# Kernel tuning notes

Measured on AMD Instinct MI355X. Metric: run time of the kernel, lower is better.

The kernel has to match this reference:

```python
import jax, jax.numpy as jnp
import numpy as np

B, D, O, K = 8192, 256, 256, 16


def setup_inputs() -> dict:
    key = jax.random.key(0)
    k1, k2, k3, k4 = jax.random.split(key, 4)
    x = jax.random.normal(k1, (B, D), dtype=jnp.float32)
    # learned params
    values = jax.random.uniform(k2, (O, D, K), dtype=jnp.float32, minval=-0.05, maxval=0.05)
    skip_w = jax.random.normal(k3, (O, D), dtype=jnp.float32) * (1.0 / np.sqrt(D))
    skip_b = jax.random.uniform(k4, (O,), dtype=jnp.float32, minval=-1.0, maxval=1.0) / np.sqrt(D)
    # fixed buffer (non-trainable)
    grid = jnp.linspace(-1.0, 1.0, K).astype(jnp.float32)
    return {"x": x, "values": values, "skip_w": skip_w, "skip_b": skip_b, "grid": grid}


def reference(x, values, skip_w, skip_b, grid):
    # x: [B, D]; values: [O, D, K]; grid: [K]
    num_knots = grid.shape[0]
    xc = jnp.clip(x, -1.0, 1.0)
    # torch.bucketize(x, grid) (right=False) == searchsorted side='left'
    right = jnp.searchsorted(grid, xc, side="left")            # [B, D]
    left = jnp.clip(right - 1, 0, num_knots - 2)               # [B, D]
    right = left + 1
    g0 = grid[left]
    g1 = grid[right]
    w = (xc - g0) / (g1 - g0 + 1e-12)                          # [B, D]
    # sparse linear-interp coefficients over knots: 2 nonzeros per (b, d)
    coeff = (1.0 - w)[..., None] * jax.nn.one_hot(left, num_knots, dtype=xc.dtype) \
          + w[..., None] * jax.nn.one_hot(right, num_knots, dtype=xc.dtype)  # [B, D, K]
    # y[b,o] = sum_d sum_k coeff[b,d,k] * values[o,d,k]  (== per-dim gather+interp+accumulate)
    y = jnp.einsum("bdk,odk->bo", coeff, values)
    y = y + xc @ skip_w.T + skip_b
    return y
```

## Files before the change

### kernel.cpp

```cpp
#include <hip/hip_runtime.h>
#include <hip/hip_bf16.h>
#include <stdint.h>


#define D_DIM  256
#define O_DIM  256
#define BM     128
#define BK     64
#define KS     4
#define ITERS  16
#define NTHR   512

typedef __attribute__((ext_vector_type(8))) short bf16x8;
typedef __attribute__((ext_vector_type(4))) float f32x4;

__global__ __launch_bounds__(256) void kan_prep(
    const float* __restrict__ values,
    const float* __restrict__ skip_w,
    const float* __restrict__ gknots,
    unsigned short* __restrict__ Vp)
{
    int tid = blockIdx.x * blockDim.x + threadIdx.x;
    int e = tid * 8;
    int o = e >> 12;
    int kflat = e & 4095;
    float sw = skip_w[(o << 8) | (kflat >> 4)];
    int kmod = kflat & 15;

    const float4* vp4 = reinterpret_cast<const float4*>(values + e);
    float4 v0 = vp4[0], v1 = vp4[1];
    float f[8] = {v0.x, v0.y, v0.z, v0.w, v1.x, v1.y, v1.z, v1.w};
    unsigned int w[4];
#pragma unroll
    for (int j = 0; j < 4; ++j) {
        float2 ab;
        ab.x = f[2*j]     + gknots[kmod + 2*j]     * sw;
        ab.y = f[2*j + 1] + gknots[kmod + 2*j + 1] * sw;
        __hip_bfloat162 p2 = __float22bfloat162_rn(ab);
        __builtin_memcpy(&w[j], &p2, 4);
    }
    size_t c = (size_t)(kflat >> 3) * 256 + (size_t)o;
    *reinterpret_cast<uint4*>(Vp + c * 8) = make_uint4(w[0], w[1], w[2], w[3]);
}

__global__ __launch_bounds__(NTHR, 2) void kan_gemm(
    const float* __restrict__ x,
    const unsigned short* __restrict__ Vp,
    float* __restrict__ part,
    float* __restrict__ out)
{
    __shared__ unsigned short As[2][BM * BK];

    const int t    = threadIdx.x;
    const int lane = t & 63;
    const int wid  = t >> 6;
    const int wm   = wid >> 2;
    const int wn   = wid & 3;
    const int l15  = lane & 15;
    const int lhi  = lane >> 4;

    const int bid = (int)blockIdx.x;
    const int m8  = bid & 7;
    const int ks  = (bid >> 3) & 3;
    const int mhi = bid >> 5;
    const int mt  = m8 + 8 * mhi;
    const int bm0 = mt * BM;
    const size_t kc0 = (size_t)ks * 128;

    const int ar = t >> 2;
    const int ad = t & 3;
    const float* xp = x + (size_t)(bm0 + ar) * D_DIM + ks * 64 + ad;

    char* arow[2] = { (char*)&As[0][0] + ar * 128, (char*)&As[1][0] + ar * 128 };
    const int ca = ((2 * ad)     ^ (ar & 7)) * 16;
    const int cb = ((2 * ad + 1) ^ (ar & 7)) * 16;

    auto stageA = [&](int buf, float xv) {
        float xc = fminf(1.f, fmaxf(-1.f, xv));
        float tt = (xc + 1.f) * 7.5f;
        int li = (int)tt;
        li = li > 14 ? 14 : li;
        float w1 = tt - (float)li;
        float2 cw; cw.x = 1.f - w1; cw.y = w1;
        __hip_bfloat162 p2 = __float22bfloat162_rn(cw);
        unsigned int pk;
        __builtin_memcpy(&pk, &p2, 4);
        unsigned long long w64 = (unsigned long long)pk << ((li & 1) * 16);
        unsigned int lo = (unsigned int)w64;
        unsigned int hi = (unsigned int)(w64 >> 32);
        int jl = li >> 1;
        unsigned int wd[8];
#pragma unroll
        for (int j = 0; j < 8; ++j)
            wd[j] = (j == jl) ? lo : ((j == jl + 1) ? hi : 0u);
        char* a = arow[buf];
        *reinterpret_cast<uint4*>(a + ca) = make_uint4(wd[0], wd[1], wd[2], wd[3]);
        *reinterpret_cast<uint4*>(a + cb) = make_uint4(wd[4], wd[5], wd[6], wd[7]);
    };

    #define LOADB(BG, KT)                                                      \
        {                                                                      \
            const unsigned short* _b =                                         \
                Vp + (kc0 + (size_t)(KT) * 8) * 2048;                          \
            _Pragma("unroll")                                                  \
            for (int kh = 0; kh < 2; ++kh)                                     \
                _Pragma("unroll")                                              \
                for (int ni = 0; ni < 4; ++ni) {                               \
                    int n = wn * 64 + ni * 16 + l15;                           \
                    BG[kh * 4 + ni] = *reinterpret_cast<const bf16x8*>(        \
                        _b + ((size_t)((kh * 4 + lhi) * 256 + n)) * 8);        \
                }                                                              \
        }

    f32x4 acc[4][4] = {};
    bf16x8 bgA[8], bgB[8];

    int abyte[4], a7[4];
#pragma unroll
    for (int mi = 0; mi < 4; ++mi) {
        int m = wm * 64 + mi * 16 + l15;
        abyte[mi] = m * 128;
        a7[mi] = m & 7;
    }

    float xnxt = xp[0];
    LOADB(bgA, 0);
    stageA(0, xnxt);
    xnxt = xp[4];
    asm volatile("s_waitcnt lgkmcnt(0)" ::: "memory");
    __builtin_amdgcn_s_barrier();
    __builtin_amdgcn_sched_barrier(0);

    #define ITERBODY(KT, CUR, BGC, BGN)                                        \
        {                                                                      \
            const bool last = (KT) == ITERS - 1;                               \
            if (!last) LOADB(BGN, (KT) + 1);                                   \
            const char* Ab = (const char*)&As[CUR][0];                         \
            bf16x8 af[4];                                                      \
                                                                   \
            _Pragma("unroll")                                                  \
            for (int mi = 0; mi < 4; ++mi)                                     \
                af[mi] = *reinterpret_cast<const bf16x8*>(                     \
                    Ab + abyte[mi] + ((lhi ^ a7[mi]) << 4));                   \
            __builtin_amdgcn_s_setprio(1);                                     \
            _Pragma("unroll")                                                  \
            for (int mi = 0; mi < 4; ++mi)                                     \
                _Pragma("unroll")                                              \
                for (int ni = 0; ni < 4; ++ni)                                 \
                    acc[mi][ni] = __builtin_amdgcn_mfma_f32_16x16x32_bf16(     \
                        af[mi], BGC[ni], acc[mi][ni], 0, 0, 0);                \
            __builtin_amdgcn_s_setprio(0);                                     \
                                      \
            if (!last) {                                                       \
                stageA((CUR) ^ 1, xnxt);                                       \
                if ((KT) + 2 < ITERS) xnxt = xp[((KT) + 2) * 4];               \
            }                                                                  \
                                                                   \
            _Pragma("unroll")                                                  \
            for (int mi = 0; mi < 4; ++mi)                                     \
                af[mi] = *reinterpret_cast<const bf16x8*>(                     \
                    Ab + abyte[mi] + (((4 + lhi) ^ a7[mi]) << 4));             \
            __builtin_amdgcn_s_setprio(1);                                     \
            _Pragma("unroll")                                                  \
            for (int mi = 0; mi < 4; ++mi)                                     \
                _Pragma("unroll")                                              \
                for (int ni = 0; ni < 4; ++ni)                                 \
                    acc[mi][ni] = __builtin_amdgcn_mfma_f32_16x16x32_bf16(     \
                        af[mi], BGC[4 + ni], acc[mi][ni], 0, 0, 0);            \
            __builtin_amdgcn_s_setprio(0);                                     \
            if (!last) {                                                       \
                asm volatile("s_waitcnt lgkmcnt(0)" ::: "memory");             \
                __builtin_amdgcn_s_barrier();                                  \
                __builtin_amdgcn_sched_barrier(0);                             \
            }                                                                  \
        }

    for (int t2 = 0; t2 < ITERS / 2; ++t2) {
        ITERBODY(2 * t2,     0, bgA, bgB);
        ITERBODY(2 * t2 + 1, 1, bgB, bgA);
    }
    #undef ITERBODY
    #undef LOADB

    float* dst = (ks == 0) ? out : part + (size_t)(ks - 1) * (8192 * 256);
#pragma unroll
    for (int ni = 0; ni < 4; ++ni) {
        int col = wn * 64 + ni * 16 + l15;
#pragma unroll
        for (int mi = 0; mi < 4; ++mi) {
            f32x4 v = acc[mi][ni];
            int row0 = bm0 + wm * 64 + mi * 16 + lhi * 4;
#pragma unroll
            for (int r = 0; r < 4; ++r)
                dst[(size_t)(row0 + r) * O_DIM + col] = v[r];
        }
    }
}

__global__ __launch_bounds__(256) void kan_reduce(
    const float* __restrict__ part,
    const float* __restrict__ skip_b,
    float* __restrict__ out)
{
    int rbid = (int)blockIdx.x;
    int c    = rbid & 7;
    int tq   = rbid >> 3;
    int mhi  = tq >> 5;
    int sub  = tq & 31;
    int mt   = c + 8 * mhi;
    int row0 = mt * BM + sub * 4;

    int i   = (int)threadIdx.x;
    int row = row0 + (i >> 6);
    int col = (i & 63) * 4;
    size_t e = (size_t)row * O_DIM + col;

    f32x4 s = *reinterpret_cast<const f32x4*>(out + e);
    s += *reinterpret_cast<const f32x4*>(skip_b + col);
    s += *reinterpret_cast<const f32x4*>(part + e);
    s += *reinterpret_cast<const f32x4*>(part + (size_t)8192 * 256 + e);
    s += *reinterpret_cast<const f32x4*>(part + (size_t)2 * 8192 * 256 + e);
    *reinterpret_cast<f32x4*>(out + e) = s;
}

__global__ __launch_bounds__(256) void kan_naive(
    const float* __restrict__ x,
    const unsigned short* __restrict__ Vp,
    const float* __restrict__ skip_b,
    float* __restrict__ out)
{
    int b = blockIdx.x, o = threadIdx.x;
    float acc = skip_b[o];
    for (int d = 0; d < 256; ++d) {
        float xc = fminf(1.f, fmaxf(-1.f, x[(size_t)b * 256 + d]));
        float tt = (xc + 1.f) * 7.5f;
        int li = (int)tt; li = li > 14 ? 14 : li;
        float w1 = tt - (float)li;
        int k0 = d * 16 + li;
        unsigned short u0 = Vp[((size_t)(k0 >> 3) * 256 + o) * 8 + (k0 & 7)];
        int k1 = k0 + 1;
        unsigned short u1 = Vp[((size_t)(k1 >> 3) * 256 + o) * 8 + (k1 & 7)];
        float f0 = __uint_as_float((unsigned)u0 << 16);
        float f1 = __uint_as_float((unsigned)u1 << 16);
        acc += (1.f - w1) * f0 + w1 * f1;
    }
    out[(size_t)b * 256 + o] = acc;
}

extern "C" void kernel_launch(void* const* d_in, const int* in_sizes, int n_in,
                              void* d_out, int out_size, void* d_ws, size_t ws_size,
                              hipStream_t stream) {
    const float* x      = (const float*)d_in[0];
    const float* values = (const float*)d_in[1];
    const float* skip_w = (const float*)d_in[2];
    const float* skip_b = (const float*)d_in[3];
    const float* gknots = (const float*)d_in[4];
    float* out = (float*)d_out;
    (void)in_sizes; (void)n_in; (void)out_size;

    unsigned short* Vp = (unsigned short*)d_ws;
    float* part = (float*)((char*)d_ws + 2u * 1024 * 1024);

    kan_prep<<<dim3(512), dim3(256), 0, stream>>>(values, skip_w, gknots, Vp);

    const size_t need = 2u * 1024 * 1024
                      + (size_t)3 * 8192 * 256 * sizeof(float);
    if (ws_size >= need) {
        kan_gemm<<<dim3(256), dim3(NTHR), 0, stream>>>(x, Vp, part, out);
        kan_reduce<<<dim3(2048), dim3(256), 0, stream>>>(part, skip_b, out);
    } else {
        kan_naive<<<dim3(8192), dim3(256), 0, stream>>>(x, Vp, skip_b, out);
    }
}
```

Before: 41.14 us.

## Stage B tiles into LDS via direct global-to-LDS loads with smaller M tiles

Halves the M tile to 64 rows with 256 threads and launches twice as many GEMM blocks. The B operand is now copied straight from global memory into double-buffered LDS with global_load_lds, replacing per-wave register loads that fetched the same B data redundantly across waves. All 16 x values are prefetched into registers at the start, and the reduce kernel's indexing is adjusted to the new tiling. The aim is fewer redundant global B reads and more blocks for occupancy, at the cost of more LDS use and extra LDS reads for B.

```diff
diff --git a/kernel.cpp b/kernel.cpp
--- a/kernel.cpp
+++ b/kernel.cpp
@@ -5,11 +5,11 @@
 
 #define D_DIM  256
 #define O_DIM  256
-#define BM     128
+#define BM     64
 #define BK     64
 #define KS     4
 #define ITERS  16
-#define NTHR   512
+#define NTHR   256
 
 typedef __attribute__((ext_vector_type(8))) short bf16x8;
 typedef __attribute__((ext_vector_type(4))) float f32x4;
@@ -50,14 +50,14 @@
     float* __restrict__ out)
 {
     __shared__ unsigned short As[2][BM * BK];
+    __shared__ unsigned short Bs[2][8 * 256 * 8];
 
     const int t    = threadIdx.x;
     const int lane = t & 63;
     const int wid  = t >> 6;
-    const int wm   = wid >> 2;
-    const int wn   = wid & 3;
     const int l15  = lane & 15;
     const int lhi  = lane >> 4;
+    const int wn64 = wid * 64;
 
     const int bid = (int)blockIdx.x;
     const int m8  = bid & 7;
@@ -68,12 +68,15 @@
     const size_t kc0 = (size_t)ks * 128;
 
     const int ar = t >> 2;
-    const int ad = t & 3;
-    const float* xp = x + (size_t)(bm0 + ar) * D_DIM + ks * 64 + ad;
+    const int dg = t & 3;
+    const float* xp = x + (size_t)(bm0 + ar) * D_DIM + ks * 64 + dg;
+    float xs[ITERS];
+#pragma unroll
+    for (int j = 0; j < ITERS; ++j) xs[j] = xp[j * 4];
 
     char* arow[2] = { (char*)&As[0][0] + ar * 128, (char*)&As[1][0] + ar * 128 };
-    const int ca = ((2 * ad)     ^ (ar & 7)) * 16;
-    const int cb = ((2 * ad + 1) ^ (ar & 7)) * 16;
+    const int ca = ((2 * dg)     ^ (ar & 7)) * 16;
+    const int cb = ((2 * dg + 1) ^ (ar & 7)) * 16;
 
     auto stageA = [&](int buf, float xv) {
         float xc = fminf(1.f, fmaxf(-1.f, xv));
@@ -98,98 +101,103 @@
         *reinterpret_cast<uint4*>(a + cb) = make_uint4(wd[4], wd[5], wd[6], wd[7]);
     };
 
-    #define LOADB(BG, KT)                                                      \
+    #define DMAB(BUF, KT)                                                      \
         {                                                                      \
-            const unsigned short* _b =                                         \
-                Vp + (kc0 + (size_t)(KT) * 8) * 2048;                          \
+            const unsigned short* _src = Vp + (kc0 + (size_t)(KT) * 8) * 2048; \
+            char* _lb = (char*)&Bs[BUF][0];                                    \
             _Pragma("unroll")                                                  \
-            for (int kh = 0; kh < 2; ++kh)                                     \
-                _Pragma("unroll")                                              \
-                for (int ni = 0; ni < 4; ++ni) {                               \
-                    int n = wn * 64 + ni * 16 + l15;                           \
-                    BG[kh * 4 + ni] = *reinterpret_cast<const bf16x8*>(        \
-                        _b + ((size_t)((kh * 4 + lhi) * 256 + n)) * 8);        \
-                }                                                              \
+            for (int j = 0; j < 8; ++j) {                                      \
+                const char* g = (const char*)(_src + (size_t)j * 2048)         \
+                                + (wn64 + lane) * 16;                          \
+                unsigned ldsoff = (unsigned)((j * 256 + wn64) * 16);           \
+                __builtin_amdgcn_global_load_lds(                              \
+                    (const __attribute__((address_space(1))) unsigned int*)g,  \
+                    (__attribute__((address_space(3))) unsigned int*)          \
+                        (_lb + ldsoff),                                        \
+                    16, 0, 0);                                                 \
+            }                                                                  \
         }
 
-    f32x4 acc[4][4] = {};
-    bf16x8 bgA[8], bgB[8];
-
     int abyte[4], a7[4];
 #pragma unroll
     for (int mi = 0; mi < 4; ++mi) {
-        int m = wm * 64 + mi * 16 + l15;
+        int m = mi * 16 + l15;
         abyte[mi] = m * 128;
         a7[mi] = m & 7;
     }
-
-    float xnxt = xp[0];
-    LOADB(bgA, 0);
-    stageA(0, xnxt);
-    xnxt = xp[4];
-    asm volatile("s_waitcnt lgkmcnt(0)" ::: "memory");
+    int bbyte[2][4];
+#pragma unroll
+    for (int kh = 0; kh < 2; ++kh)
+#pragma unroll
+        for (int ni = 0; ni < 4; ++ni)
+            bbyte[kh][ni] = (((kh * 4 + lhi) * 256) + wn64 + ni * 16 + l15) * 16;
+
+    f32x4 acc[4][4] = {};
+
+    DMAB(0, 0)
+    stageA(0, xs[0]);
+    asm volatile("s_waitcnt vmcnt(0) lgkmcnt(0)" ::: "memory");
     __builtin_amdgcn_s_barrier();
     __builtin_amdgcn_sched_barrier(0);
 
-    #define ITERBODY(KT, CUR, BGC, BGN)                                        \
+    #define IT(KT, CUR)                                                        \
         {                                                                      \
-            const bool last = (KT) == ITERS - 1;                               \
-            if (!last) LOADB(BGN, (KT) + 1);                                   \
+            if ((KT) + 1 < ITERS) {                                            \
+                DMAB((CUR) ^ 1, (KT) + 1)                                      \
+                asm volatile("s_waitcnt vmcnt(8)" ::: "memory");               \
+            } else {                                                           \
+                asm volatile("s_waitcnt vmcnt(0)" ::: "memory");               \
+            }                                                                  \
+            __builtin_amdgcn_sched_barrier(0);                                 \
             const char* Ab = (const char*)&As[CUR][0];                         \
-            bf16x8 af[4];                                                      \
-                                                                   \
+            const char* Bb = (const char*)&Bs[CUR][0];                         \
+            bf16x8 af[4][2], bg[4][2];                                         \
             _Pragma("unroll")                                                  \
-            for (int mi = 0; mi < 4; ++mi)                                     \
-                af[mi] = *reinterpret_cast<const bf16x8*>(                     \
-                    Ab + abyte[mi] + ((lhi ^ a7[mi]) << 4));                   \
+            for (int kh = 0; kh < 2; ++kh) {                                   \
+                int k8 = kh * 4 + lhi;                                         \
+                _Pragma("unroll")                                              \
+                for (int mi = 0; mi < 4; ++mi)                                 \
+                    af[mi][kh] = *reinterpret_cast<const bf16x8*>(             \
+                        Ab + abyte[mi] + ((k8 ^ a7[mi]) << 4));                \
+                _Pragma("unroll")                                              \
+                for (int ni = 0; ni < 4; ++ni)                                 \
+                    bg[ni][kh] = *reinterpret_cast<const bf16x8*>(             \
+                        Bb + bbyte[kh][ni]);                                   \
+            }                                                                  \
+            if ((KT) + 1 < ITERS) stageA((CUR) ^ 1, xs[(KT) + 1 < ITERS ?     \
+                                                       (KT) + 1 : 0]);         \
             __builtin_amdgcn_s_setprio(1);                                     \
             _Pragma("unroll")                                                  \
             for (int mi = 0; mi < 4; ++mi)                                     \
                 _Pragma("unroll")                                              \
                 for (int ni = 0; ni < 4; ++ni)                                 \
-                    acc[mi][ni] = __builtin_amdgcn_mfma_f32_16x16x32_bf16(     \
-                        af[mi], BGC[ni], acc[mi][ni], 0, 0, 0);                \
+                    _Pragma("unroll")                                          \
+                    for (int kh = 0; kh < 2; ++kh)                             \
+                        acc[mi][ni] = __builtin_amdgcn_mfma_f32_16x16x32_bf16( \
+                            af[mi][kh], bg[ni][kh], acc[mi][ni], 0, 0, 0);     \
             __builtin_amdgcn_s_setprio(0);                                     \
-                                      \
-            if (!last) {                                                       \
-                stageA((CUR) ^ 1, xnxt);                                       \
-                if ((KT) + 2 < ITERS) xnxt = xp[((KT) + 2) * 4];               \
-            }                                                                  \
-                                                                   \
-            _Pragma("unroll")                                                  \
-            for (int mi = 0; mi < 4; ++mi)                                     \
-                af[mi] = *reinterpret_cast<const bf16x8*>(                     \
-                    Ab + abyte[mi] + (((4 + lhi) ^ a7[mi]) << 4));             \
-            __builtin_amdgcn_s_setprio(1);                                     \
-            _Pragma("unroll")                                                  \
-            for (int mi = 0; mi < 4; ++mi)                                     \
-                _Pragma("unroll")                                              \
-                for (int ni = 0; ni < 4; ++ni)                                 \
-                    acc[mi][ni] = __builtin_amdgcn_mfma_f32_16x16x32_bf16(     \
-                        af[mi], BGC[4 + ni], acc[mi][ni], 0, 0, 0);            \
-            __builtin_amdgcn_s_setprio(0);                                     \
-            if (!last) {                                                       \
+            if ((KT) + 1 < ITERS) {                                            \
                 asm volatile("s_waitcnt lgkmcnt(0)" ::: "memory");             \
                 __builtin_amdgcn_s_barrier();                                  \
                 __builtin_amdgcn_sched_barrier(0);                             \
             }                                                                  \
         }
 
-    for (int t2 = 0; t2 < ITERS / 2; ++t2) {
-        ITERBODY(2 * t2,     0, bgA, bgB);
-        ITERBODY(2 * t2 + 1, 1, bgB, bgA);
-    }
-    #undef ITERBODY
-    #undef LOADB
+    IT(0, 0)   IT(1, 1)   IT(2, 0)   IT(3, 1)
+    IT(4, 0)   IT(5, 1)   IT(6, 0)   IT(7, 1)
+    IT(8, 0)   IT(9, 1)   IT(10, 0)  IT(11, 1)
+    IT(12, 0)  IT(13, 1)  IT(14, 0)  IT(15, 1)
+    #undef IT
+    #undef DMAB
 
     float* dst = (ks == 0) ? out : part + (size_t)(ks - 1) * (8192 * 256);
 #pragma unroll
     for (int ni = 0; ni < 4; ++ni) {
-        int col = wn * 64 + ni * 16 + l15;
+        int col = wn64 + ni * 16 + l15;
 #pragma unroll
         for (int mi = 0; mi < 4; ++mi) {
             f32x4 v = acc[mi][ni];
-            int row0 = bm0 + wm * 64 + mi * 16 + lhi * 4;
+            int row0 = bm0 + mi * 16 + lhi * 4;
 #pragma unroll
             for (int r = 0; r < 4; ++r)
                 dst[(size_t)(row0 + r) * O_DIM + col] = v[r];
@@ -205,8 +213,8 @@
     int rbid = (int)blockIdx.x;
     int c    = rbid & 7;
     int tq   = rbid >> 3;
-    int mhi  = tq >> 5;
-    int sub  = tq & 31;
+    int mhi  = tq >> 4;
+    int sub  = tq & 15;
     int mt   = c + 8 * mhi;
     int row0 = mt * BM + sub * 4;
 
@@ -266,7 +274,7 @@
     const size_t need = 2u * 1024 * 1024
                       + (size_t)3 * 8192 * 256 * sizeof(float);
     if (ws_size >= need) {
-        kan_gemm<<<dim3(256), dim3(NTHR), 0, stream>>>(x, Vp, part, out);
+        kan_gemm<<<dim3(512), dim3(NTHR), 0, stream>>>(x, Vp, part, out);
         kan_reduce<<<dim3(2048), dim3(256), 0, stream>>>(part, skip_b, out);
     } else {
         kan_naive<<<dim3(8192), dim3(256), 0, stream>>>(x, Vp, skip_b, out);
```

New measurement: 41.53 us. About the same (+0.9%).

## Deepen B register prefetch to two stages and warm x into cache in prep

Applied to the files above, without the earlier changes.

The GEMM main loop now keeps three rotating B-fragment register sets and issues global loads two k-steps ahead instead of one, so more memory latency is hidden behind the MFMA work. The prep kernel also reads the x rows that each GEMM block will later use and discards the sum, pulling x into L2 before the GEMM runs. The deeper prefetch adds eight more bf16x8 registers per thread, which may hurt occupancy under the 2-blocks launch bound. The cache warm-up adds extra reads to the prep kernel.

```diff
diff --git a/kernel.cpp b/kernel.cpp
--- a/kernel.cpp
+++ b/kernel.cpp
@@ -18,6 +18,7 @@
     const float* __restrict__ values,
     const float* __restrict__ skip_w,
     const float* __restrict__ gknots,
+    const float* __restrict__ x,
     unsigned short* __restrict__ Vp)
 {
     int tid = blockIdx.x * blockDim.x + threadIdx.x;
@@ -41,6 +42,22 @@
     }
     size_t c = (size_t)(kflat >> 3) * 256 + (size_t)o;
     *reinterpret_cast<uint4*>(Vp + c * 8) = make_uint4(w[0], w[1], w[2], w[3]);
+
+    {
+        int pb = (int)blockIdx.x;
+        int mt = (pb & 7) + 8 * ((pb >> 3) & 7);
+        int rowbase = mt * BM + (pb >> 6) * 16;
+        int t = (int)threadIdx.x;
+        const float4* xw = reinterpret_cast<const float4*>(
+            x + (size_t)(rowbase + (t >> 4)) * D_DIM) + (t & 15) * 4;
+        float s = 0.f;
+#pragma unroll
+        for (int k = 0; k < 4; ++k) {
+            float4 v = xw[k];
+            s += v.x + v.y + v.z + v.w;
+        }
+        asm volatile("" :: "v"(s));
+    }
 }
 
 __global__ __launch_bounds__(NTHR, 2) void kan_gemm(
@@ -113,7 +130,7 @@
         }
 
     f32x4 acc[4][4] = {};
-    bf16x8 bgA[8], bgB[8];
+    bf16x8 bgA[8], bgB[8], bgC[8];
 
     int abyte[4], a7[4];
 #pragma unroll
@@ -124,17 +141,18 @@
     }
 
     float xnxt = xp[0];
-    LOADB(bgA, 0);
+    LOADB(bgA, 0)
+    LOADB(bgB, 1)
     stageA(0, xnxt);
     xnxt = xp[4];
     asm volatile("s_waitcnt lgkmcnt(0)" ::: "memory");
     __builtin_amdgcn_s_barrier();
     __builtin_amdgcn_sched_barrier(0);
 
-    #define ITERBODY(KT, CUR, BGC, BGN)                                        \
+    #define IT(KT, CUR, BGC_, BGN2)                                            \
         {                                                                      \
             const bool last = (KT) == ITERS - 1;                               \
-            if (!last) LOADB(BGN, (KT) + 1);                                   \
+            if ((KT) + 2 < ITERS) { LOADB(BGN2, (KT) + 2) }                    \
             const char* Ab = (const char*)&As[CUR][0];                         \
             bf16x8 af[4];                                                      \
                                                                    \
@@ -148,7 +166,7 @@
                 _Pragma("unroll")                                              \
                 for (int ni = 0; ni < 4; ++ni)                                 \
                     acc[mi][ni] = __builtin_amdgcn_mfma_f32_16x16x32_bf16(     \
-                        af[mi], BGC[ni], acc[mi][ni], 0, 0, 0);                \
+                        af[mi], BGC_[ni], acc[mi][ni], 0, 0, 0);               \
             __builtin_amdgcn_s_setprio(0);                                     \
                                       \
             if (!last) {                                                       \
@@ -166,7 +184,7 @@
                 _Pragma("unroll")                                              \
                 for (int ni = 0; ni < 4; ++ni)                                 \
                     acc[mi][ni] = __builtin_amdgcn_mfma_f32_16x16x32_bf16(     \
-                        af[mi], BGC[4 + ni], acc[mi][ni], 0, 0, 0);            \
+                        af[mi], BGC_[4 + ni], acc[mi][ni], 0, 0, 0);           \
             __builtin_amdgcn_s_setprio(0);                                     \
             if (!last) {                                                       \
                 asm volatile("s_waitcnt lgkmcnt(0)" ::: "memory");             \
@@ -175,11 +193,13 @@
             }                                                                  \
         }
 
-    for (int t2 = 0; t2 < ITERS / 2; ++t2) {
-        ITERBODY(2 * t2,     0, bgA, bgB);
-        ITERBODY(2 * t2 + 1, 1, bgB, bgA);
-    }
-    #undef ITERBODY
+    IT(0, 0, bgA, bgC)  IT(1, 1, bgB, bgA)  IT(2, 0, bgC, bgB)
+    IT(3, 1, bgA, bgC)  IT(4, 0, bgB, bgA)  IT(5, 1, bgC, bgB)
+    IT(6, 0, bgA, bgC)  IT(7, 1, bgB, bgA)  IT(8, 0, bgC, bgB)
+    IT(9, 1, bgA, bgC)  IT(10, 0, bgB, bgA) IT(11, 1, bgC, bgB)
+    IT(12, 0, bgA, bgC) IT(13, 1, bgB, bgA) IT(14, 0, bgC, bgB)
+    IT(15, 1, bgA, bgC)
+    #undef IT
     #undef LOADB
 
     float* dst = (ks == 0) ? out : part + (size_t)(ks - 1) * (8192 * 256);
@@ -261,7 +281,7 @@
     unsigned short* Vp = (unsigned short*)d_ws;
     float* part = (float*)((char*)d_ws + 2u * 1024 * 1024);
 
-    kan_prep<<<dim3(512), dim3(256), 0, stream>>>(values, skip_w, gknots, Vp);
+    kan_prep<<<dim3(512), dim3(256), 0, stream>>>(values, skip_w, gknots, x, Vp);
 
     const size_t need = 2u * 1024 * 1024
                       + (size_t)3 * 8192 * 256 * sizeof(float);
```

Measured after the change: 40.27 us. -2.1%, faster.
